# Performance work log

Measured on AMD Instinct MI355X. Metric: run time of the kernel, lower is better.

The kernel has to match this reference:

```python
import jax, jax.numpy as jnp
import numpy as np

B, T, V, E, H, L = 64, 512, 100, 100, 256, 8


def _lstm_layer(xs, w_ih, w_hh, b_ih, b_hh):
    # xs: [B, T, I]; PyTorch gate order: i, f, g, o
    gx = jnp.einsum('bti,gi->btg', xs, w_ih) + b_ih  # [B, T, 4H]
    gx = jnp.swapaxes(gx, 0, 1)                      # [T, B, 4H]
    w_hh_t = w_hh.T                                  # [H, 4H]
    h0 = jnp.zeros((xs.shape[0], w_hh.shape[1]), xs.dtype)

    def step(carry, g):
        h, c = carry
        g = g + h @ w_hh_t + b_hh
        i, f, gg, o = jnp.split(g, 4, axis=-1)
        c = jax.nn.sigmoid(f) * c + jax.nn.sigmoid(i) * jnp.tanh(gg)
        h = jax.nn.sigmoid(o) * jnp.tanh(c)
        return (h, c), h

    (hT, cT), ys = jax.lax.scan(step, (h0, h0), gx)
    return jnp.swapaxes(ys, 0, 1), hT, cT


def setup_inputs() -> dict:
    key = jax.random.key(0)
    ks = jax.random.split(key, 9)
    s = 0.05  # roughly PyTorch's 1/sqrt(H) uniform scale
    return {
        'x': jax.random.randint(ks[0], (B, T), 0, V),
        'embed': jax.random.normal(ks[1], (V, E), jnp.float32) * s,
        'w_ih0': jax.random.normal(ks[2], (4 * H, E), jnp.float32) * s,
        'w_ih': jax.random.normal(ks[3], (L - 1, 4 * H, H), jnp.float32) * s,
        'w_hh': jax.random.normal(ks[4], (L, 4 * H, H), jnp.float32) * s,
        'b_ih': jax.random.normal(ks[5], (L, 4 * H), jnp.float32) * s,
        'b_hh': jax.random.normal(ks[6], (L, 4 * H), jnp.float32) * s,
        'fc_w': jax.random.normal(ks[7], (V, H), jnp.float32) * s,
        'fc_b': jax.random.normal(ks[8], (V,), jnp.float32) * s,
    }


def reference(x, embed, w_ih0, w_ih, w_hh, b_ih, b_hh, fc_w, fc_b):
    h = embed[x]  # [B, T, E]
    h_fin, c_fin = [], []
    for l in range(L):
        wih = w_ih0 if l == 0 else w_ih[l - 1]
        h, hT, cT = _lstm_layer(h, wih, w_hh[l], b_ih[l], b_hh[l])
        h_fin.append(hT)
        c_fin.append(cT)
    logits = jnp.einsum('bth,vh->btv', h, fc_w) + fc_b  # [B, T, V]
    return logits, jnp.stack(h_fin), jnp.stack(c_fin)
```

## Files before the change

kernel.cpp:

```cpp
#include <hip/hip_runtime.h>


typedef _Float16 f16;
typedef f16  f16x8 __attribute__((ext_vector_type(8)));
typedef f16  f16x4 __attribute__((ext_vector_type(4)));
typedef float f32x4 __attribute__((ext_vector_type(4)));
typedef int   i32x4 __attribute__((ext_vector_type(4)));

#define DEV __device__ __forceinline__

constexpr int TT = 512, BB = 64, VV = 100, HH = 256, LL = 8;
constexpr int RING_D = 32;

constexpr size_t XE_OFF = 0;
constexpr size_t XE_SZ  = (size_t)TT*BB*256*2;
constexpr size_t WP_OFF = XE_OFF + XE_SZ;
constexpr size_t WP_SZ  = (size_t)LL*16*64*512*2;
constexpr size_t BI_OFF = WP_OFF + WP_SZ;
constexpr size_t BI_SZ  = (size_t)LL*16*64*4;
constexpr size_t FW_OFF = BI_OFF + BI_SZ;
constexpr size_t FW_SZ  = (size_t)112*256*2;
constexpr size_t H7_OFF = FW_OFF + FW_SZ;
constexpr size_t H7_SZ  = (size_t)TT*BB*256*2;
constexpr size_t RG_OFF = H7_OFF + H7_SZ;
constexpr size_t RG_SZ  = (size_t)LL*RING_D*BB*256*2;
constexpr size_t FPF_OFF = RG_OFF + RG_SZ;
constexpr size_t FPF_SZ  = (size_t)LL*TT*16;
constexpr size_t FCF_OFF = FPF_OFF + FPF_SZ;
constexpr size_t FCF_SZ  = (size_t)7*TT*16;
constexpr int ZERO_DW = (int)((FPF_SZ + FCF_SZ) / 4);

DEV void ld16_pl (i32x4& d, const void* p){ asm volatile("global_load_dwordx4 %0, %1, off"     : "=v"(d) : "v"(p)); }
DEV void ld16_sc1(i32x4& d, const void* p){ asm volatile("global_load_dwordx4 %0, %1, off sc1" : "=v"(d) : "v"(p)); }
DEV void st16_sc1(void* p, i32x4 d){ asm volatile("global_store_dwordx4 %0, %1, off sc1" :: "v"(p), "v"(d) : "memory"); }
DEV void stb_sc1(void* p){ unsigned o = 1; asm volatile("global_store_byte %0, %1, off sc1" :: "v"(p), "v"(o) : "memory"); }
DEV void wait_vm0(){ asm volatile("s_waitcnt vmcnt(0)" ::: "memory"); __builtin_amdgcn_sched_barrier(0); }
DEV void wait_vm8(){ asm volatile("s_waitcnt vmcnt(8)" ::: "memory"); __builtin_amdgcn_sched_barrier(0); }

DEV bool pollw0(const unsigned char* ph, const unsigned char* px,
                const unsigned char* pc, int ln) {
  const unsigned char* pa = (ln == 0) ? ph : (ln == 1) ? px : (ln == 2) ? pc : nullptr;
  for (int it = 0; it < (1 << 16); ++it) {
    bool ok = true;
    if (pa) {
      i32x4 f;
      asm volatile("global_load_dwordx4 %0, %1, off sc1\n\ts_waitcnt vmcnt(0)"
                   : "=v"(f) : "v"(pa) : "memory");
      ok = ((f[0] & f[1] & f[2] & f[3]) == 0x01010101);
    }
    if (__all(ok)) return true;
  }
  return false;
}

DEV float sig2(float y)  { return __builtin_amdgcn_rcpf(1.f + __builtin_amdgcn_exp2f(-y)); }
DEV float tanhp(float y) { return 1.f - 2.f * __builtin_amdgcn_rcpf(1.f + __builtin_amdgcn_exp2f(y)); }
constexpr float LOG2E = 1.4426950408889634f;
constexpr float C2LE  = 2.8853900817779268f;
DEV unsigned f16bits(float v) { f16 h = (f16)v; return (unsigned)__builtin_bit_cast(unsigned short, h); }

__global__ void prep_zero(unsigned int* p) {
  p[blockIdx.x * 256 + threadIdx.x] = 0;
}

__global__ void prep_embed(const int* __restrict__ x, const float* __restrict__ em,
                           f16* __restrict__ xe) {
  int g = blockIdx.x * 256 + threadIdx.x;
  int chunk = g & 7, pair = g >> 3;
  int b = pair & 63, t = pair >> 6;
  int idx = x[b * 512 + t];
  const float* er = em + (size_t)idx * 100;
  f16* o = xe + (size_t)pair * 256 + chunk * 32;
  #pragma unroll
  for (int c4 = 0; c4 < 32; c4 += 4) {
    f16x4 v;
    #pragma unroll
    for (int q = 0; q < 4; ++q) {
      int c = chunk * 32 + c4 + q;
      v[q] = (c < 100) ? (f16)er[c] : (f16)0.f;
    }
    *(f16x4*)(o + c4) = v;
  }
}

__global__ void prep_w(const float* __restrict__ w_ih0, const float* __restrict__ w_ih,
                       const float* __restrict__ w_hh, f16* __restrict__ wpo) {
  int g = blockIdx.x * 256 + threadIdx.x;
  int k4 = (g & 127) * 4;
  int n  = (g >> 7) & 63;
  int ls = g >> 13;
  int l = ls >> 4, s = ls & 15;
  int gate = n & 3;
  int u = s * 16 + ((n >> 4) << 2) + ((n >> 2) & 3);
  int r = 256 * gate + u;
  float scale = (gate == 2) ? C2LE : LOG2E;
  f16x4 v;
  #pragma unroll
  for (int q = 0; q < 4; ++q) {
    int k = k4 + q;
    float f;
    if (k < 256) {
      if (l == 0) f = (k < 100) ? w_ih0[(size_t)r * 100 + k] : 0.f;
      else        f = w_ih[((size_t)(l - 1) * 1024 + r) * 256 + k];
    } else        f = w_hh[((size_t)l * 1024 + r) * 256 + (k - 256)];
    v[q] = (f16)(f * scale);
  }
  *(f16x4*)(wpo + (size_t)g * 4) = v;
}

__global__ void prep_bias(const float* __restrict__ b_ih, const float* __restrict__ b_hh,
                          float* __restrict__ bo) {
  int g = blockIdx.x * 256 + threadIdx.x;
  int n = g & 63, s = (g >> 6) & 15, l = g >> 10;
  int gate = n & 3;
  int u = s * 16 + ((n >> 4) << 2) + ((n >> 2) & 3);
  int r = 256 * gate + u;
  float scale = (gate == 2) ? C2LE : LOG2E;
  bo[g] = (b_ih[l * 1024 + r] + b_hh[l * 1024 + r]) * scale;
}

__global__ void prep_fcw(const float* __restrict__ fc_w, f16* __restrict__ fo) {
  int g = blockIdx.x * 256 + threadIdx.x;
  int n = g >> 6, k4 = (g & 63) * 4;
  f16x4 v;
  #pragma unroll
  for (int q = 0; q < 4; ++q)
    v[q] = (n < 100) ? (f16)fc_w[(size_t)n * 256 + k4 + q] : (f16)0.f;
  *(f16x4*)(fo + (size_t)g * 4) = v;
}

__global__ void __launch_bounds__(512, 1) lstm_pipe(
    const f16* __restrict__ xe, const f16* __restrict__ wp, const float* __restrict__ biasp,
    f16* h7, f16* rings, unsigned char* fpf, unsigned char* fcf, float* out)
{
  __shared__ char pad_lds[40960];
  __shared__ unsigned short pub[2][64][24];
  (void)((volatile char*)pad_lds)[threadIdx.x];

  const int bx  = blockIdx.x;
  const int lyr = bx & 7;
  const int sl  = bx >> 3;
  const int tid = threadIdx.x;
  const int wv  = tid >> 6;
  const int ln  = tid & 63;
  const int mA  = wv >> 2;
  const int nB  = wv & 3;

  f16x8 wfa[2][16];
  {
    const f16* wb = wp + (size_t)(lyr * 16 + sl) * 64 * 512;
    #pragma unroll
    for (int tt = 0; tt < 2; ++tt)
      #pragma unroll
      for (int kt = 0; kt < 16; ++kt) {
        wfa[tt][kt] = *(const f16x8*)(wb + (size_t)((2 * mA + tt) * 16 + (ln & 15)) * 512
                                      + kt * 32 + (ln >> 4) * 8);
        i32x4 pin = __builtin_bit_cast(i32x4, wfa[tt][kt]);
        asm volatile("" : "+v"(pin));
        wfa[tt][kt] = __builtin_bit_cast(f16x8, pin);
      }
  }
  f32x4 bias_v[2];
  #pragma unroll
  for (int tt = 0; tt < 2; ++tt) {
    bias_v[tt] = *(const f32x4*)(biasp + (size_t)(lyr * 16 + sl) * 64
                                 + (2 * mA + tt) * 16 + (ln >> 4) * 4);
    asm volatile("" : "+v"(bias_v[tt]));
  }

  float cst0 = 0.f, cst1 = 0.f;
  const int q    = ln >> 4;
  const int bcol = nB * 16 + (ln & 15);
  const int kof  = q * 8;
  const f16* xring = rings + (size_t)(lyr - 1) * RING_D * 16384;
  f16*       hring = rings + (size_t)lyr * RING_D * 16384;
  bool dead = false;

  for (int t = 0; t < TT; ++t) {
    if (wv == 0 && !dead) {
      const unsigned char* ph = (t > 0)   ? fpf + (size_t)(lyr * TT + (t - 1)) * 16 : nullptr;
      const unsigned char* px = (lyr > 0) ? fpf + (size_t)((lyr - 1) * TT + t) * 16 : nullptr;
      const unsigned char* pc = (lyr < 7 && t >= RING_D)
                                ? fcf + (size_t)(lyr * TT + (t - RING_D)) * 16 : nullptr;
      dead = !pollw0(ph, px, pc, ln);
    }
    __syncthreads();

    const bool hasH = (t > 0);
    i32x4 bfx[8], bfh[8];
    {
      const f16* xb = ((lyr == 0) ? xe + (size_t)t * 16384
                                  : xring + (size_t)(t & (RING_D - 1)) * 16384)
                      + (size_t)bcol * 256 + kof;
      if (lyr == 0) {
        #pragma unroll
        for (int kt = 0; kt < 8; ++kt) ld16_pl(bfx[kt], xb + kt * 32);
      } else {
        #pragma unroll
        for (int kt = 0; kt < 8; ++kt) ld16_sc1(bfx[kt], xb + kt * 32);
      }
      if (hasH) {
        const f16* hb = hring + (size_t)((t - 1) & (RING_D - 1)) * 16384
                      + (size_t)bcol * 256 + kof;
        #pragma unroll
        for (int kt = 0; kt < 8; ++kt) ld16_sc1(bfh[kt], hb + kt * 32);
      }
    }

    f32x4 acc0 = {0,0,0,0}, acc1 = {0,0,0,0};
    if (hasH) wait_vm8(); else wait_vm0();
    #pragma unroll
    for (int kt = 0; kt < 8; ++kt) {
      f16x8 av = __builtin_bit_cast(f16x8, bfx[kt]);
      acc0 = __builtin_amdgcn_mfma_f32_16x16x32_f16(wfa[0][kt], av, acc0, 0, 0, 0);
      acc1 = __builtin_amdgcn_mfma_f32_16x16x32_f16(wfa[1][kt], av, acc1, 0, 0, 0);
    }
    if (hasH) {
      wait_vm0();
      #pragma unroll
      for (int kt = 0; kt < 8; ++kt) {
        f16x8 av = __builtin_bit_cast(f16x8, bfh[kt]);
        acc0 = __builtin_amdgcn_mfma_f32_16x16x32_f16(wfa[0][8 + kt], av, acc0, 0, 0, 0);
        acc1 = __builtin_amdgcn_mfma_f32_16x16x32_f16(wfa[1][8 + kt], av, acc1, 0, 0, 0);
      }
    }

    const int par = t & 1;
    #pragma unroll
    for (int tt = 0; tt < 2; ++tt) {
      f32x4 g4 = (tt == 0 ? acc0 : acc1);
      g4 += bias_v[tt];
      float i_ = sig2(g4[0]), f_ = sig2(g4[1]), z_ = tanhp(g4[2]), o_ = sig2(g4[3]);
      float& c_ = (tt == 0 ? cst0 : cst1);
      c_ = f_ * c_ + i_ * z_;
      float h_ = o_ * tanhp(c_ * C2LE);
      pub[par][bcol][(2 * mA + tt) * 4 + q] = (unsigned short)f16bits(h_);
      if (t == TT - 1) {
        const int u = sl * 16 + (2 * mA + tt) * 4 + q;
        size_t ob = 3276800 + (size_t)lyr * 16384 + (size_t)bcol * 256 + u;
        out[ob] = h_;  out[ob + 131072] = c_;
      }
    }
    __syncthreads();

    if (wv == 0) {
      i32x4 d0 = *(const i32x4*)&pub[par][ln][0];
      i32x4 d1 = *(const i32x4*)&pub[par][ln][8];
      f16* dst = hring + (size_t)(t & (RING_D - 1)) * 16384 + (size_t)ln * 256 + sl * 16;
      st16_sc1(dst, d0);
      st16_sc1(dst + 8, d1);
      if (lyr == 7) {
        f16* hd = h7 + (size_t)t * 16384 + (size_t)ln * 256 + sl * 16;
        *(i32x4*)hd = d0;
        *(i32x4*)(hd + 8) = d1;
      }
      wait_vm0();
      if (ln == 0) stb_sc1(fpf + (size_t)(lyr * TT + t) * 16 + sl);
      if (ln == 1 && lyr > 0)
        stb_sc1(fcf + (size_t)((lyr - 1) * TT + t) * 16 + sl);
    }
  }
}

__global__ void __launch_bounds__(256, 1) fc_kernel(
    const f16* __restrict__ h7, const f16* __restrict__ fcw,
    const float* __restrict__ fcb, float* __restrict__ out)
{
  const int t  = blockIdx.x;
  const int wv = threadIdx.x >> 6;
  const int ln = threadIdx.x & 63;
  const f16* ab = h7 + (size_t)t * 16384 + (size_t)(wv * 16 + (ln & 15)) * 256 + (ln >> 4) * 8;
  f16x8 af[8];
  #pragma unroll
  for (int kt = 0; kt < 8; ++kt) af[kt] = *(const f16x8*)(ab + kt * 32);
  const int obrow = wv * 16 + (ln >> 4) * 4;
  #pragma unroll
  for (int nt = 0; nt < 7; ++nt) {
    const f16* bb = fcw + (size_t)(nt * 16 + (ln & 15)) * 256 + (ln >> 4) * 8;
    f32x4 acc = {0, 0, 0, 0};
    #pragma unroll
    for (int kt = 0; kt < 8; ++kt) {
      f16x8 bv = *(const f16x8*)(bb + kt * 32);
      acc = __builtin_amdgcn_mfma_f32_16x16x32_f16(af[kt], bv, acc, 0, 0, 0);
    }
    int vg = nt * 16 + (ln & 15);
    if (vg < VV) {
      float bias = fcb[vg];
      #pragma unroll
      for (int j = 0; j < 4; ++j)
        out[(size_t)(obrow + j) * 51200 + (size_t)t * 100 + vg] = acc[j] + bias;
    }
  }
}

extern "C" void kernel_launch(void* const* d_in, const int* in_sizes, int n_in,
                              void* d_out, int out_size, void* d_ws, size_t ws_size,
                              hipStream_t stream) {
  (void)in_sizes; (void)n_in; (void)out_size; (void)ws_size;
  const int*   x     = (const int*)d_in[0];
  const float* embed = (const float*)d_in[1];
  const float* w_ih0 = (const float*)d_in[2];
  const float* w_ih  = (const float*)d_in[3];
  const float* w_hh  = (const float*)d_in[4];
  const float* b_ih  = (const float*)d_in[5];
  const float* b_hh  = (const float*)d_in[6];
  const float* fc_w  = (const float*)d_in[7];
  const float* fc_b  = (const float*)d_in[8];
  char* ws = (char*)d_ws;
  float* out = (float*)d_out;

  prep_zero<<<120, 256, 0, stream>>>((unsigned int*)(ws + FPF_OFF));
  prep_embed<<<1024, 256, 0, stream>>>(x, embed, (f16*)(ws + XE_OFF));
  prep_w<<<4096, 256, 0, stream>>>(w_ih0, w_ih, w_hh, (f16*)(ws + WP_OFF));
  prep_bias<<<32, 256, 0, stream>>>(b_ih, b_hh, (float*)(ws + BI_OFF));
  prep_fcw<<<28, 256, 0, stream>>>(fc_w, (f16*)(ws + FW_OFF));

  lstm_pipe<<<128, 512, 35072, stream>>>(
      (const f16*)(ws + XE_OFF), (const f16*)(ws + WP_OFF), (const float*)(ws + BI_OFF),
      (f16*)(ws + H7_OFF), (f16*)(ws + RG_OFF),
      (unsigned char*)(ws + FPF_OFF), (unsigned char*)(ws + FCF_OFF), out);

  fc_kernel<<<512, 256, 0, stream>>>((const f16*)(ws + H7_OFF), (const f16*)(ws + FW_OFF),
                                     fc_b, out);
}
```

Baseline: 2.948 ms.

## Replace per-step flag polling with poison-sentinel data validation in ring buffers

Removes the per-timestep produced flags and the block-wide poll+syncthreads. Consumers now load h and x directly from the ring buffers and retry when they see an f16 infinity poison sentinel, which producers write into the next slot ahead of time. This removes a flag round trip and a barrier from the critical recurrent path. The price is a retry loop, the poison pre-fill, and a correctness risk: the scheme relies on store ordering between the poison write and the later data write, and a real value equal to the sentinel would stall the consumer.

```diff
diff --git a/kernel.cpp b/kernel.cpp
--- a/kernel.cpp
+++ b/kernel.cpp
@@ -11,6 +11,8 @@
 
 constexpr int TT = 512, BB = 64, VV = 100, HH = 256, LL = 8;
 constexpr int RING_D = 32;
+constexpr int POISON = 0x7C007C00;
+constexpr int MAXRETRY = 4096;
 
 constexpr size_t XE_OFF = 0;
 constexpr size_t XE_SZ  = (size_t)TT*BB*256*2;
@@ -24,11 +26,8 @@
 constexpr size_t H7_SZ  = (size_t)TT*BB*256*2;
 constexpr size_t RG_OFF = H7_OFF + H7_SZ;
 constexpr size_t RG_SZ  = (size_t)LL*RING_D*BB*256*2;
-constexpr size_t FPF_OFF = RG_OFF + RG_SZ;
-constexpr size_t FPF_SZ  = (size_t)LL*TT*16;
-constexpr size_t FCF_OFF = FPF_OFF + FPF_SZ;
+constexpr size_t FCF_OFF = RG_OFF + RG_SZ;
 constexpr size_t FCF_SZ  = (size_t)7*TT*16;
-constexpr int ZERO_DW = (int)((FPF_SZ + FCF_SZ) / 4);
 
 DEV void ld16_pl (i32x4& d, const void* p){ asm volatile("global_load_dwordx4 %0, %1, off"     : "=v"(d) : "v"(p)); }
 DEV void ld16_sc1(i32x4& d, const void* p){ asm volatile("global_load_dwordx4 %0, %1, off sc1" : "=v"(d) : "v"(p)); }
@@ -37,18 +36,25 @@
 DEV void wait_vm0(){ asm volatile("s_waitcnt vmcnt(0)" ::: "memory"); __builtin_amdgcn_sched_barrier(0); }
 DEV void wait_vm8(){ asm volatile("s_waitcnt vmcnt(8)" ::: "memory"); __builtin_amdgcn_sched_barrier(0); }
 
-DEV bool pollw0(const unsigned char* ph, const unsigned char* px,
-                const unsigned char* pc, int ln) {
-  const unsigned char* pa = (ln == 0) ? ph : (ln == 1) ? px : (ln == 2) ? pc : nullptr;
+DEV bool chk8(const i32x4* f) {
+  int bad = 0;
+  #pragma unroll
+  for (int i = 0; i < 8; ++i) {
+    bad |= (f[i][0] == POISON);
+    bad |= (f[i][1] == POISON);
+    bad |= (f[i][2] == POISON);
+    bad |= (f[i][3] == POISON);
+  }
+  return __all(bad == 0);
+}
+
+DEV bool poll16(const unsigned char* p) {
   for (int it = 0; it < (1 << 16); ++it) {
-    bool ok = true;
-    if (pa) {
-      i32x4 f;
-      asm volatile("global_load_dwordx4 %0, %1, off sc1\n\ts_waitcnt vmcnt(0)"
-                   : "=v"(f) : "v"(pa) : "memory");
-      ok = ((f[0] & f[1] & f[2] & f[3]) == 0x01010101);
-    }
-    if (__all(ok)) return true;
+    i32x4 f;
+    asm volatile("global_load_dwordx4 %0, %1, off sc1\n\ts_waitcnt vmcnt(0)"
+                 : "=v"(f) : "v"(p) : "memory");
+    if ((f[0] & f[1] & f[2] & f[3]) == 0x01010101) return true;
+    if (it > 2) __builtin_amdgcn_s_sleep(1);
   }
   return false;
 }
@@ -61,6 +67,11 @@
 
 __global__ void prep_zero(unsigned int* p) {
   p[blockIdx.x * 256 + threadIdx.x] = 0;
+}
+__global__ void prep_poison(unsigned int* p) {
+  size_t i = ((size_t)blockIdx.x * 256 + threadIdx.x) * 4;
+  i32x4 P = {POISON, POISON, POISON, POISON};
+  *(i32x4*)(p + i) = P;
 }
 
 __global__ void prep_embed(const int* __restrict__ x, const float* __restrict__ em,
@@ -131,7 +142,7 @@
 
 __global__ void __launch_bounds__(512, 1) lstm_pipe(
     const f16* __restrict__ xe, const f16* __restrict__ wp, const float* __restrict__ biasp,
-    f16* h7, f16* rings, unsigned char* fpf, unsigned char* fcf, float* out)
+    f16* h7, f16* rings, unsigned char* fcf, float* out)
 {
   __shared__ char pad_lds[40960];
   __shared__ unsigned short pub[2][64][24];
@@ -177,14 +188,15 @@
   bool dead = false;
 
   for (int t = 0; t < TT; ++t) {
-    if (wv == 0 && !dead) {
-      const unsigned char* ph = (t > 0)   ? fpf + (size_t)(lyr * TT + (t - 1)) * 16 : nullptr;
-      const unsigned char* px = (lyr > 0) ? fpf + (size_t)((lyr - 1) * TT + t) * 16 : nullptr;
-      const unsigned char* pc = (lyr < 7 && t >= RING_D)
-                                ? fcf + (size_t)(lyr * TT + (t - RING_D)) * 16 : nullptr;
-      dead = !pollw0(ph, px, pc, ln);
-    }
-    __syncthreads();
+    if (wv == 0 && t + 1 < TT) {
+      if (lyr < 7 && t + 1 >= RING_D && !dead)
+        dead = !poll16(fcf + (size_t)(lyr * TT + (t + 1 - RING_D)) * 16);
+      f16* pz = hring + (size_t)((t + 1) & (RING_D - 1)) * 16384
+              + (size_t)ln * 256 + sl * 16;
+      i32x4 P = {POISON, POISON, POISON, POISON};
+      st16_sc1(pz, P);
+      st16_sc1(pz + 8, P);
+    }
 
     const bool hasH = (t > 0);
     i32x4 bfx[8], bfh[8];
@@ -206,17 +218,42 @@
         for (int kt = 0; kt < 8; ++kt) ld16_sc1(bfh[kt], hb + kt * 32);
       }
     }
+    if (hasH) wait_vm8(); else wait_vm0();
+
+    if (lyr > 0 && !dead) {
+      int it = 0;
+      while (!chk8(bfx)) {
+        if (++it > MAXRETRY) { dead = true; break; }
+        wait_vm0();
+        const f16* xb = xring + (size_t)(t & (RING_D - 1)) * 16384
+                      + (size_t)bcol * 256 + kof;
+        #pragma unroll
+        for (int kt = 0; kt < 8; ++kt) ld16_sc1(bfx[kt], xb + kt * 32);
+        wait_vm0();
+      }
+    }
 
     f32x4 acc0 = {0,0,0,0}, acc1 = {0,0,0,0};
-    if (hasH) wait_vm8(); else wait_vm0();
     #pragma unroll
     for (int kt = 0; kt < 8; ++kt) {
       f16x8 av = __builtin_bit_cast(f16x8, bfx[kt]);
       acc0 = __builtin_amdgcn_mfma_f32_16x16x32_f16(wfa[0][kt], av, acc0, 0, 0, 0);
       acc1 = __builtin_amdgcn_mfma_f32_16x16x32_f16(wfa[1][kt], av, acc1, 0, 0, 0);
     }
+
     if (hasH) {
       wait_vm0();
+      if (!dead) {
+        int it = 0;
+        while (!chk8(bfh)) {
+          if (++it > MAXRETRY) { dead = true; break; }
+          const f16* hb = hring + (size_t)((t - 1) & (RING_D - 1)) * 16384
+                        + (size_t)bcol * 256 + kof;
+          #pragma unroll
+          for (int kt = 0; kt < 8; ++kt) ld16_sc1(bfh[kt], hb + kt * 32);
+          wait_vm0();
+        }
+      }
       #pragma unroll
       for (int kt = 0; kt < 8; ++kt) {
         f16x8 av = __builtin_bit_cast(f16x8, bfh[kt]);
@@ -254,8 +291,6 @@
         *(i32x4*)hd = d0;
         *(i32x4*)(hd + 8) = d1;
       }
-      wait_vm0();
-      if (ln == 0) stb_sc1(fpf + (size_t)(lyr * TT + t) * 16 + sl);
       if (ln == 1 && lyr > 0)
         stb_sc1(fcf + (size_t)((lyr - 1) * TT + t) * 16 + sl);
     }
@@ -309,7 +344,8 @@
   char* ws = (char*)d_ws;
   float* out = (float*)d_out;
 
-  prep_zero<<<120, 256, 0, stream>>>((unsigned int*)(ws + FPF_OFF));
+  prep_zero<<<56, 256, 0, stream>>>((unsigned int*)(ws + FCF_OFF));
+  prep_poison<<<2048, 256, 0, stream>>>((unsigned int*)(ws + RG_OFF));
   prep_embed<<<1024, 256, 0, stream>>>(x, embed, (f16*)(ws + XE_OFF));
   prep_w<<<4096, 256, 0, stream>>>(w_ih0, w_ih, w_hh, (f16*)(ws + WP_OFF));
   prep_bias<<<32, 256, 0, stream>>>(b_ih, b_hh, (float*)(ws + BI_OFF));
@@ -318,7 +354,7 @@
   lstm_pipe<<<128, 512, 35072, stream>>>(
       (const f16*)(ws + XE_OFF), (const f16*)(ws + WP_OFF), (const float*)(ws + BI_OFF),
       (f16*)(ws + H7_OFF), (f16*)(ws + RG_OFF),
-      (unsigned char*)(ws + FPF_OFF), (unsigned char*)(ws + FCF_OFF), out);
+      (unsigned char*)(ws + FCF_OFF), out);
 
   fc_kernel<<<512, 256, 0, stream>>>((const f16*)(ws + H7_OFF), (const f16*)(ws + FW_OFF),
                                      fc_b, out);
```

After: 3.117 ms. 1.06x slower.
